# Kernel tuning notes

Hardware: AMD Instinct MI355X
Metric: run time of the kernel (lower is better)

## Reference

```python
import jax, jax.numpy as jnp
import numpy as np

N_NODES = 100000
N_EDGES = 800000
VOCAB = 256      # node_dict_size
NODE_DIM = 256
HIDDEN = 256
N_MASK = 10000


def setup_inputs() -> dict:
    key = jax.random.key(0)
    ks = jax.random.split(key, 8)
    return {
        "x": jax.random.randint(ks[0], (N_NODES, 1), 0, VOCAB, dtype=jnp.int64 if jax.config.jax_enable_x64 else jnp.int32),
        "edge_index": jax.random.randint(ks[1], (2, N_EDGES), 0, N_NODES, dtype=jnp.int32),
        "mask_x_position": jax.random.randint(ks[2], (N_MASK,), 0, N_NODES, dtype=jnp.int32),
        "emb": jax.random.normal(ks[3], (VOCAB, NODE_DIM), dtype=jnp.float32) * (NODE_DIM ** -0.5),
        "W1": jax.random.normal(ks[4], (NODE_DIM, HIDDEN), dtype=jnp.float32) * (NODE_DIM ** -0.5),
        "b1": jnp.zeros((HIDDEN,), dtype=jnp.float32),
        "W2": jax.random.normal(ks[5], (HIDDEN, VOCAB), dtype=jnp.float32) * (HIDDEN ** -0.5),
        "b2": jnp.zeros((VOCAB,), dtype=jnp.float32),
    }


def _gcn_conv(h, W, b, src, dst, norm, n_nodes):
    # PyG GCNConv: out = scatter_add(norm * (h @ W)[src], dst) + b
    hw = h @ W                                      # [N, out]
    msgs = hw[src] * norm[:, None]                  # [E+N, out]
    out = jax.ops.segment_sum(msgs, dst, num_segments=n_nodes)
    return out + b


def _gcn_norm(edge_index, n_nodes):
    # add self-loops, compute sym-normalized edge weights (PyG gcn_norm)
    loops = jnp.arange(n_nodes, dtype=edge_index.dtype)
    src = jnp.concatenate([edge_index[0], loops])
    dst = jnp.concatenate([edge_index[1], loops])
    deg = jax.ops.segment_sum(jnp.ones_like(dst, dtype=jnp.float32), dst,
                              num_segments=n_nodes)  # in-degree incl. self-loop
    dinv = jnp.where(deg > 0, jax.lax.rsqrt(deg), 0.0)
    norm = dinv[src] * dinv[dst]                    # [E+N]
    return src, dst, norm


def reference(x, edge_index, mask_x_position, emb, W1, b1, W2, b2):
    n_nodes = x.shape[0]
    src, dst, norm = _gcn_norm(edge_index, n_nodes)
    h = emb[x[:, 0]]                                # Embedding + squeeze(1) -> [N, node_dim]
    # dropout p=0 / eval mode -> identity
    h = _gcn_conv(h, W1, b1, src, dst, norm, n_nodes)
    h = jax.nn.relu(h)
    h = _gcn_conv(h, W2, b2, src, dst, norm, n_nodes)  # [N, vocab]
    return jax.nn.log_softmax(h[mask_x_position], axis=1)
```

## Files before the change

kernel.cpp:

```cpp
#include <hip/hip_runtime.h>
#include <stdint.h>

#define NN 100000
#define NE 800000
#define ND 256
#define NM 10000
#define NMP 10048
#define NPB 256
#define NBK 391
#define BCAP 2560
#define TILE 4096
#define EBK ((NE + TILE - 1) / TILE)

typedef __attribute__((ext_vector_type(8))) short bf16x8;
typedef __attribute__((ext_vector_type(4))) float f32x4;

__device__ __forceinline__ float bf2f(unsigned short u) {
    return __uint_as_float(((unsigned)u) << 16);
}
__device__ __forceinline__ unsigned short f2bf(float f) {
    unsigned u = __float_as_uint(f);
    u += 0x7fffu + ((u >> 16) & 1u);
    return (unsigned short)(u >> 16);
}


__global__ void k_maskmap(const int* __restrict__ mpos, int* __restrict__ minfo,
                          unsigned char* __restrict__ mb, unsigned char* __restrict__ fb,
                          int* __restrict__ gcur, int* __restrict__ nctr) {
    int j = blockIdx.x * 256 + threadIdx.x;
    if (j < NM) {
        int p = mpos[j];
        minfo[p] = (j + 1) << 1;
        mb[p] = 1;
        fb[p] = 1;
    }
    if (j < NBK) gcur[j << 4] = j * BCAP;
    if (j == 0) *nctr = 0;
}

__global__ __launch_bounds__(1024) void k_bin(
    const int* __restrict__ src, const int* __restrict__ dst,
    const unsigned char* __restrict__ mb, unsigned char* __restrict__ fb,
    int* __restrict__ gcur, int* __restrict__ ebuf,
    const float* __restrict__ emb, const float* __restrict__ W1,
    const float* __restrict__ W2,
    unsigned short* __restrict__ M1, unsigned short* __restrict__ W2t) {
    __shared__ int lcnt[NBK];
    __shared__ int sd[TILE], ss[TILE];
    __shared__ float er4[4 * ND];
    int b = blockIdx.x, t = threadIdx.x;
    if (b >= EBK) {
        int bb = b - EBK;
        int row = t >> 8, col = t & 255;
        if (bb < 64) {
            er4[t] = emb[(bb * 4) * ND + t];
            __syncthreads();
            float acc = 0.f;
            for (int k = 0; k < ND; k++) acc += er4[row * ND + k] * W1[k * ND + col];
            M1[(bb * 4 + row) * ND + col] = f2bf(acc);
        } else {
            int n = (bb - 64) * 4 + row;
            W2t[n * ND + col] = f2bf(W2[col * ND + n]);
        }
        return;
    }
    for (int i = t; i < NBK; i += 1024) lcnt[i] = 0;
    __syncthreads();
    int e0 = b * TILE;
#pragma unroll
    for (int k = 0; k < TILE / 1024; k++) {
        int idx = t + k * 1024;
        int e = e0 + idx;
        if (e < NE) {
            int d = dst[e], s = src[e];
            sd[idx] = d; ss[idx] = s;
            atomicAdd(&lcnt[d >> 8], 1);
            if (mb[d] == 1) fb[s] = 1;
        }
    }
    __syncthreads();
    for (int i = t; i < NBK; i += 1024) {
        int c = lcnt[i];
        lcnt[i] = c ? atomicAdd(&gcur[i << 4], c) : 0;
    }
    __syncthreads();
    int nv = min(NE - e0, TILE);
#pragma unroll
    for (int k = 0; k < TILE / 1024; k++) {
        int idx = t + k * 1024;
        if (idx < nv) {
            int d = sd[idx], s = ss[idx];
            int bk = d >> 8, j = d & 255;
            int pos = atomicAdd(&lcnt[bk], 1);
            if (pos < (bk + 1) * BCAP) ebuf[pos] = s | (j << 17);
        }
    }
}

__global__ void k_bhist(const int* __restrict__ gcur, const int* __restrict__ ebuf,
                        const int* __restrict__ x, const unsigned char* __restrict__ mb,
                        const unsigned char* __restrict__ fb,
                        int* __restrict__ carr, int4* __restrict__ xd4,
                        int* __restrict__ nctr, int* __restrict__ part) {
    __shared__ int bins[NPB];
    __shared__ int rs[4];
    int b = blockIdx.x, t = threadIdx.x;
    int lane = t & 63, wv = t >> 6;
    bins[t] = 0;
    __syncthreads();
    int n = min(gcur[b << 4] - b * BCAP, BCAP);
    int base = b * BCAP;
    for (int i = t; i < n; i += 256)
        atomicAdd(&bins[ebuf[base + i] >> 17], 1);
    __syncthreads();
    int node = b * NPB + t;
    int w = 0;
    if (node < NN) {
        int c = bins[t];
        carr[node] = c;
        float dv = rsqrtf((float)c + 1.0f);
        int cc = 0;
        if (fb[node] == 1) cc = atomicAdd(nctr, 1);
        xd4[node] = make_int4(x[node], __float_as_int(dv), cc, 0);
        w = c + ((mb[node] == 1) ? c : 0);
    }
#pragma unroll
    for (int o = 32; o >= 1; o >>= 1) w += __shfl_xor(w, o, 64);
    if (lane == 0) rs[wv] = w;
    __syncthreads();
    if (t == 0) part[b] = rs[0] + rs[1] + rs[2] + rs[3];
}

__global__ __launch_bounds__(256) void k_place(
    const int* __restrict__ gcur, const int* __restrict__ ebuf,
    const int* __restrict__ minfo, const unsigned char* __restrict__ fb,
    const int* __restrict__ carr, const int* __restrict__ part,
    const int4* __restrict__ xd4, int* __restrict__ off, int2* __restrict__ pairs,
    int4* __restrict__ nrec) {
    __shared__ int sinfo[NPB], lc1[NPB], lc2[NPB];
    __shared__ int bred[4], wtot[4];
    int b = blockIdx.x, t = threadIdx.x;
    int lane = t & 63, wv = t >> 6;
    int pv = 0;
    for (int i = t; i < b; i += 256) pv += part[i];
#pragma unroll
    for (int o = 32; o >= 1; o >>= 1) pv += __shfl_xor(pv, o, 64);
    if (lane == 0) bred[wv] = pv;
    __syncthreads();
    int pbase = bred[0] + bred[1] + bred[2] + bred[3];
    int node = b * NPB + t;
    int c = 0, m = 0, f = 0;
    if (node < NN) {
        c = carr[node];
        int mv = minfo[node];
        if (mv > 0) m = mv;
        f = (fb[node] == 1) ? 1 : 0;
    }
    int wgt = c + (m ? c : 0);
    int xx = wgt;
    for (int o = 1; o < 64; o <<= 1) { int y = __shfl_up(xx, o, 64); if (lane >= o) xx += y; }
    if (lane == 63) wtot[wv] = xx;
    __syncthreads();
    int wadd = 0;
#pragma unroll
    for (int k = 0; k < 4; k++) if (k < wv) wadd += wtot[k];
    int excl = xx - wgt + wadd;
    int myoff = pbase + excl;
    if (node < NN) {
        off[node] = myoff;
        if (f) {
            int4 xv = xd4[node];
            nrec[xv.z] = make_int4(xv.x, xv.y, myoff, c);
        }
    }
    sinfo[t] = m | f;
    lc1[t] = myoff;
    lc2[t] = myoff + c;
    __syncthreads();
    int n = min(gcur[b << 4] - b * BCAP, BCAP);
    int base = b * BCAP;
    for (int i = t; i < n; i += 256) {
        int w = ebuf[base + i];
        int j = w >> 17, s = w & 0x1FFFF;
        int ii = sinfo[j];
        if (ii == 0) continue;
        int4 xv = xd4[s];
        if (ii & 1) {
            int p = atomicAdd(&lc1[j], 1);
            pairs[p] = make_int2(xv.x, xv.y);
        }
        if (ii > 1) {
            int p = atomicAdd(&lc2[j], 1);
            pairs[p] = make_int2(xv.z, xv.y);
        }
    }
}

__global__ __launch_bounds__(1024) void k_expand(
    const int* __restrict__ nctr, const int4* __restrict__ nrec,
    const int2* __restrict__ pairs,
    const unsigned short* __restrict__ M1,
    const float* __restrict__ b1,
    unsigned short* __restrict__ h1c) {
    __shared__ unsigned short sm1[ND * ND];
    int t = threadIdx.x;
    {
        const uint4* g = (const uint4*)M1;
        uint4* s = (uint4*)sm1;
        for (int i = t; i < (ND * ND) / 8; i += 1024) s[i] = g[i];
    }
    __syncthreads();
    int lane = t & 63;
    float4 b1v = ((const float4*)b1)[lane];
    int nw = nctr[0];
    for (int idx = (blockIdx.x * 1024 + t) >> 6; idx < nw; idx += 4096) {
        int4 rec = nrec[idx];
        int v0 = rec.x;
        float w0 = __int_as_float(rec.y);
        ushort4 mm = *(const ushort4*)(sm1 + v0 * ND + lane * 4);
        float a0 = w0 * bf2f(mm.x), a1 = w0 * bf2f(mm.y);
        float a2 = w0 * bf2f(mm.z), a3 = w0 * bf2f(mm.w);
        int e = rec.z, end = e + rec.w;
        for (; e + 4 <= end; e += 4) {
            int2 pA = pairs[e + 0];
            int2 pB = pairs[e + 1];
            int2 pC = pairs[e + 2];
            int2 pD = pairs[e + 3];
            ushort4 mA = *(const ushort4*)(sm1 + pA.x * ND + lane * 4);
            ushort4 mB = *(const ushort4*)(sm1 + pB.x * ND + lane * 4);
            ushort4 mC = *(const ushort4*)(sm1 + pC.x * ND + lane * 4);
            ushort4 mD = *(const ushort4*)(sm1 + pD.x * ND + lane * 4);
            float wA = __int_as_float(pA.y), wB = __int_as_float(pB.y);
            float wC = __int_as_float(pC.y), wD = __int_as_float(pD.y);
            a0 += wA * bf2f(mA.x) + wB * bf2f(mB.x) + wC * bf2f(mC.x) + wD * bf2f(mD.x);
            a1 += wA * bf2f(mA.y) + wB * bf2f(mB.y) + wC * bf2f(mC.y) + wD * bf2f(mD.y);
            a2 += wA * bf2f(mA.z) + wB * bf2f(mB.z) + wC * bf2f(mC.z) + wD * bf2f(mD.z);
            a3 += wA * bf2f(mA.w) + wB * bf2f(mB.w) + wC * bf2f(mC.w) + wD * bf2f(mD.w);
        }
        for (; e < end; e++) {
            int2 p = pairs[e];
            float w = __int_as_float(p.y);
            ushort4 m2 = *(const ushort4*)(sm1 + p.x * ND + lane * 4);
            a0 += w * bf2f(m2.x);
            a1 += w * bf2f(m2.y);
            a2 += w * bf2f(m2.z);
            a3 += w * bf2f(m2.w);
        }
        ushort4 o;
        o.x = f2bf(fmaxf(fmaf(w0, a0, b1v.x), 0.f));
        o.y = f2bf(fmaxf(fmaf(w0, a1, b1v.y), 0.f));
        o.z = f2bf(fmaxf(fmaf(w0, a2, b1v.z), 0.f));
        o.w = f2bf(fmaxf(fmaf(w0, a3, b1v.w), 0.f));
        ((ushort4*)(h1c + (size_t)idx * ND))[lane] = o;
    }
}

__global__ void k_agg2(const int* __restrict__ mpos, const int* __restrict__ minfo,
                       const int4* __restrict__ xd4,
                       const int2* __restrict__ pairs, const int* __restrict__ off,
                       const int* __restrict__ carr,
                       const unsigned short* __restrict__ h1c,
                       unsigned short* __restrict__ agg2b) {
    int lane = threadIdx.x & 63;
    int wave = (blockIdx.x * 256 + threadIdx.x) >> 6;
    if (wave >= NM) return;
    int r = wave;
    int p = mpos[r];
    if ((minfo[p] >> 1) != r + 1) return;
    int4 xp = xd4[p];
    int cp = xp.z;
    float dv = __int_as_float(xp.y);
    ushort4 h0 = *(const ushort4*)(h1c + (size_t)cp * ND + lane * 4);
    float a0 = dv * bf2f(h0.x), a1 = dv * bf2f(h0.y);
    float a2 = dv * bf2f(h0.z), a3 = dv * bf2f(h0.w);
    int c2 = carr[p];
    int e = off[p] + c2, end = e + c2;
    for (; e + 4 <= end; e += 4) {
        int2 pA = pairs[e + 0];
        int2 pB = pairs[e + 1];
        int2 pC = pairs[e + 2];
        int2 pD = pairs[e + 3];
        ushort4 hA = *(const ushort4*)(h1c + (size_t)pA.x * ND + lane * 4);
        ushort4 hB = *(const ushort4*)(h1c + (size_t)pB.x * ND + lane * 4);
        ushort4 hC = *(const ushort4*)(h1c + (size_t)pC.x * ND + lane * 4);
        ushort4 hD = *(const ushort4*)(h1c + (size_t)pD.x * ND + lane * 4);
        float wA = __int_as_float(pA.y), wB = __int_as_float(pB.y);
        float wC = __int_as_float(pC.y), wD = __int_as_float(pD.y);
        a0 += wA * bf2f(hA.x) + wB * bf2f(hB.x) + wC * bf2f(hC.x) + wD * bf2f(hD.x);
        a1 += wA * bf2f(hA.y) + wB * bf2f(hB.y) + wC * bf2f(hC.y) + wD * bf2f(hD.y);
        a2 += wA * bf2f(hA.z) + wB * bf2f(hB.z) + wC * bf2f(hC.z) + wD * bf2f(hD.z);
        a3 += wA * bf2f(hA.w) + wB * bf2f(hB.w) + wC * bf2f(hC.w) + wD * bf2f(hD.w);
    }
    for (; e < end; e++) {
        int2 pp = pairs[e];
        float w = __int_as_float(pp.y);
        ushort4 hv = *(const ushort4*)(h1c + (size_t)pp.x * ND + lane * 4);
        a0 += w * bf2f(hv.x);
        a1 += w * bf2f(hv.y);
        a2 += w * bf2f(hv.z);
        a3 += w * bf2f(hv.w);
    }
    ushort4 o;
    o.x = f2bf(dv * a0);
    o.y = f2bf(dv * a1);
    o.z = f2bf(dv * a2);
    o.w = f2bf(dv * a3);
    ((ushort4*)(agg2b + (size_t)r * ND))[lane] = o;
}

__global__ __launch_bounds__(256) void k_out2(
    const int* __restrict__ mpos, const int* __restrict__ minfo,
    const unsigned short* __restrict__ agg2b, const unsigned short* __restrict__ W2t,
    const float* __restrict__ b2, float* __restrict__ out) {
    int lane = threadIdx.x & 63;
    int wv = threadIdx.x >> 6;
    int row0 = blockIdx.x * 64 + wv * 16;
    int qm = lane & 15, qk = lane >> 4;
    int row = row0 + qm;
    bf16x8 afr[8];
    if (row < NM) {
        int p = mpos[row];
        int rr = (minfo[p] >> 1) - 1;
        const unsigned short* arow = agg2b + (size_t)rr * ND + qk * 8;
#pragma unroll
        for (int kt = 0; kt < 8; kt++) afr[kt] = *(const bf16x8*)(arow + kt * 32);
    } else {
#pragma unroll
        for (int kt = 0; kt < 8; kt++) afr[kt] = (bf16x8){0, 0, 0, 0, 0, 0, 0, 0};
    }
    f32x4 acc[16];
#pragma unroll
    for (int t = 0; t < 16; t++) acc[t] = (f32x4){0.f, 0.f, 0.f, 0.f};
#pragma unroll
    for (int t = 0; t < 16; t++) {
        const unsigned short* brow = W2t + (size_t)(t * 16 + qm) * ND + qk * 8;
#pragma unroll
        for (int kt = 0; kt < 8; kt++) {
            bf16x8 bfr = *(const bf16x8*)(brow + kt * 32);
            acc[t] = __builtin_amdgcn_mfma_f32_16x16x32_bf16(afr[kt], bfr, acc[t], 0, 0, 0);
        }
    }
    float mx[4] = {-1e30f, -1e30f, -1e30f, -1e30f};
#pragma unroll
    for (int t = 0; t < 16; t++) {
        float cb = b2[qm + 16 * t];
#pragma unroll
        for (int r = 0; r < 4; r++) {
            float v = acc[t][r] + cb;
            acc[t][r] = v;
            mx[r] = fmaxf(mx[r], v);
        }
    }
#pragma unroll
    for (int r = 0; r < 4; r++)
        for (int o = 1; o < 16; o <<= 1) mx[r] = fmaxf(mx[r], __shfl_xor(mx[r], o, 64));
    float sm[4] = {0.f, 0.f, 0.f, 0.f};
#pragma unroll
    for (int t = 0; t < 16; t++)
#pragma unroll
        for (int r = 0; r < 4; r++) sm[r] += __expf(acc[t][r] - mx[r]);
#pragma unroll
    for (int r = 0; r < 4; r++)
        for (int o = 1; o < 16; o <<= 1) sm[r] += __shfl_xor(sm[r], o, 64);
#pragma unroll
    for (int r = 0; r < 4; r++) {
        int orow_i = row0 + qk * 4 + r;
        if (orow_i >= NM) continue;
        float lse = mx[r] + __logf(sm[r]);
        float* orow = out + (size_t)orow_i * ND + qm;
#pragma unroll
        for (int t = 0; t < 16; t++) orow[16 * t] = acc[t][r] - lse;
    }
}

extern "C" void kernel_launch(void* const* d_in, const int* in_sizes, int n_in,
                              void* d_out, int out_size, void* d_ws, size_t ws_size,
                              hipStream_t stream) {
    const int* x    = (const int*)d_in[0];
    const int* ei   = (const int*)d_in[1];
    const int* src  = ei;
    const int* dst  = ei + NE;
    const int* mpos = (const int*)d_in[2];
    const float* emb = (const float*)d_in[3];
    const float* W1  = (const float*)d_in[4];
    const float* b1  = (const float*)d_in[5];
    const float* W2  = (const float*)d_in[6];
    const float* b2  = (const float*)d_in[7];
    float* out = (float*)d_out;

    char* w = (char*)d_ws;
    size_t o = 0;
#define ALLOC(nbytes) ({ void* _p = (void*)(w + o); o = (o + (size_t)(nbytes) + 63) & ~(size_t)63; _p; })
    int*   carr  = (int*)ALLOC((size_t)(NN + 64) * 4);
    int*   off   = (int*)ALLOC((size_t)(NN + 64) * 4);
    int*   minfo = (int*)ALLOC((size_t)NN * 4);
    unsigned char* mb = (unsigned char*)ALLOC(NN + 64);
    unsigned char* fb = (unsigned char*)ALLOC(NN + 64);
    int4*  xd4   = (int4*)ALLOC((size_t)NN * 16);
    int*   nctr  = (int*)ALLOC(64);
    int*   part  = (int*)ALLOC(512 * 4);
    int*   gcur  = (int*)ALLOC((size_t)(NBK * 16 + 64) * 4);
    int*   ebuf  = (int*)ALLOC((size_t)NBK * BCAP * 4);
    unsigned short* M1    = (unsigned short*)ALLOC((size_t)ND * ND * 2);
    unsigned short* W2t   = (unsigned short*)ALLOC((size_t)ND * ND * 2);
    unsigned short* agg2b = (unsigned short*)ALLOC((size_t)NM * ND * 2);
    int2*  pairs = (int2*)ALLOC((size_t)NE * 2 * 8);
    int4*  nrec  = (int4*)ALLOC((size_t)NN * 16);
    unsigned short* h1c  = (unsigned short*)ALLOC((size_t)NN * ND * 2);
#undef ALLOC

    k_maskmap<<<(NM + 255) / 256, 256, 0, stream>>>(mpos, minfo, mb, fb, gcur, nctr);
    k_bin<<<EBK + 128, 1024, 0, stream>>>(src, dst, mb, fb, gcur, ebuf,
                                          emb, W1, W2, M1, W2t);
    k_bhist<<<NBK, 256, 0, stream>>>(gcur, ebuf, x, mb, fb, carr, xd4, nctr, part);
    k_place<<<NBK, 256, 0, stream>>>(gcur, ebuf, minfo, fb, carr, part, xd4, off, pairs, nrec);
    k_expand<<<256, 1024, 0, stream>>>(nctr, nrec, pairs, M1, b1, h1c);
    k_agg2<<<(NM + 3) / 4, 256, 0, stream>>>(mpos, minfo, xd4, pairs, off, carr, h1c, agg2b);
    k_out2<<<NMP / 64, 256, 0, stream>>>(mpos, minfo, agg2b, W2t, b2, out);
}
```

Before: 190.0 us.

## Locally sort edges by bucket in LDS before coalesced scatter to global bins

The binning kernel now prefix-sums the per-bucket counts within each block and places every edge into a shared-memory staging array ordered by bucket. It then writes the staged entries to global ebuf in index order, so consecutive threads write contiguous runs and the global stores coalesce better than scattered per-edge writes. The cost is re-reading src/dst from global memory in the second pass instead of caching them, plus an extra scan and more synchronisation barriers.

```diff
diff --git a/kernel.cpp b/kernel.cpp
--- a/kernel.cpp
+++ b/kernel.cpp
@@ -46,10 +46,12 @@
     const float* __restrict__ emb, const float* __restrict__ W1,
     const float* __restrict__ W2,
     unsigned short* __restrict__ M1, unsigned short* __restrict__ W2t) {
-    __shared__ int lcnt[NBK];
-    __shared__ int sd[TILE], ss[TILE];
+    __shared__ int lcnt[NBK], lstart[NBK], delta[NBK], cur[NBK];
+    __shared__ int sv[TILE], sgd[TILE];
+    __shared__ int wsum[8], wpre[8];
     __shared__ float er4[4 * ND];
     int b = blockIdx.x, t = threadIdx.x;
+    int lane = t & 63, wv = t >> 6;
     if (b >= EBK) {
         int bb = b - EBK;
         int row = t >> 8, col = t & 255;
@@ -68,33 +70,61 @@
     for (int i = t; i < NBK; i += 1024) lcnt[i] = 0;
     __syncthreads();
     int e0 = b * TILE;
+    int nv = min(NE - e0, TILE);
 #pragma unroll
     for (int k = 0; k < TILE / 1024; k++) {
-        int idx = t + k * 1024;
-        int e = e0 + idx;
+        int e = e0 + t + k * 1024;
+        if (e < NE) {
+            int d = dst[e];
+            atomicAdd(&lcnt[d >> 8], 1);
+            if (mb[d] == 1) fb[src[e]] = 1;
+        }
+    }
+    __syncthreads();
+    {
+        int v = 0;
+        if (t < 448) {
+            v = (t < NBK) ? lcnt[t] : 0;
+            int incl = v;
+            for (int o = 1; o < 64; o <<= 1) {
+                int y = __shfl_up(incl, o, 64);
+                if (lane >= o) incl += y;
+            }
+            if (lane == 63) wsum[wv] = incl;
+            if (t < NBK) lstart[t] = incl - v;
+        }
+        __syncthreads();
+        if (t == 0) {
+            int s = 0;
+            for (int k = 0; k < 7; k++) { wpre[k] = s; s += wsum[k]; }
+        }
+        __syncthreads();
+        if (t < NBK) {
+            int ls = lstart[t] + wpre[wv];
+            lstart[t] = ls;
+            int c = v;
+            int gpos = c ? atomicAdd(&gcur[t << 4], c) : 0;
+            delta[t] = gpos - ls;
+            cur[t] = ls;
+        }
+    }
+    __syncthreads();
+#pragma unroll
+    for (int k = 0; k < TILE / 1024; k++) {
+        int e = e0 + t + k * 1024;
         if (e < NE) {
             int d = dst[e], s = src[e];
-            sd[idx] = d; ss[idx] = s;
-            atomicAdd(&lcnt[d >> 8], 1);
-            if (mb[d] == 1) fb[s] = 1;
-        }
-    }
-    __syncthreads();
-    for (int i = t; i < NBK; i += 1024) {
-        int c = lcnt[i];
-        lcnt[i] = c ? atomicAdd(&gcur[i << 4], c) : 0;
-    }
-    __syncthreads();
-    int nv = min(NE - e0, TILE);
-#pragma unroll
-    for (int k = 0; k < TILE / 1024; k++) {
-        int idx = t + k * 1024;
-        if (idx < nv) {
-            int d = sd[idx], s = ss[idx];
-            int bk = d >> 8, j = d & 255;
-            int pos = atomicAdd(&lcnt[bk], 1);
-            if (pos < (bk + 1) * BCAP) ebuf[pos] = s | (j << 17);
-        }
+            int bk = d >> 8;
+            int r = atomicAdd(&cur[bk], 1);
+            int gp = delta[bk] + r;
+            sv[r] = s | ((d & 255) << 17);
+            sgd[r] = (gp < (bk + 1) * BCAP) ? gp : -1;
+        }
+    }
+    __syncthreads();
+    for (int i = t; i < nv; i += 1024) {
+        int gp = sgd[i];
+        if (gp >= 0) ebuf[gp] = sv[i];
     }
 }
 
```

Result: no change. 188.5 us, median of 2 (-0.8%).
